# Kernel tuning notes

Hardware: AMD Instinct MI355X
Metric: run time of the kernel (lower is better)

Reference implementation:

```python
import jax, jax.numpy as jnp
import numpy as np

D_MODEL = 1024
NUM_HEADS = 16
D_K = D_MODEL // NUM_HEADS


def setup_inputs() -> dict:
    key = jax.random.key(0)
    ks = jax.random.split(key, 12)
    b, t1, t2 = 4, 2048, 2048
    s = 1.0 / np.sqrt(D_MODEL)
    inp = {
        "q": jax.random.normal(ks[0], (b, t1, D_MODEL), jnp.float32),
        "k": jax.random.normal(ks[1], (b, t2, D_MODEL), jnp.float32),
        "v": jax.random.normal(ks[2], (b, t2, D_MODEL), jnp.float32),
        "mask": jnp.ones((b, 1, 1, t2), dtype=bool),
        "w_q": jax.random.normal(ks[3], (D_MODEL, D_MODEL), jnp.float32) * s,
        "b_q": jax.random.normal(ks[4], (D_MODEL,), jnp.float32) * s,
        "w_k": jax.random.normal(ks[5], (D_MODEL, D_MODEL), jnp.float32) * s,
        "b_k": jax.random.normal(ks[6], (D_MODEL,), jnp.float32) * s,
        "w_v": jax.random.normal(ks[7], (D_MODEL, D_MODEL), jnp.float32) * s,
        "b_v": jax.random.normal(ks[8], (D_MODEL,), jnp.float32) * s,
        "w_o": jax.random.normal(ks[9], (D_MODEL, D_MODEL), jnp.float32) * s,
        "b_o": jax.random.normal(ks[10], (D_MODEL,), jnp.float32) * s,
    }
    return inp


def reference(q, k, v, mask, w_q, b_q, w_k, b_k, w_v, b_v, w_o, b_o):
    b, t1, _ = q.shape
    t2 = k.shape[1]
    # projections -> (b, h, t, d_k)
    qh = (q @ w_q.T + b_q).reshape(b, t1, NUM_HEADS, D_K).transpose(0, 2, 1, 3)
    kh = (k @ w_k.T + b_k).reshape(b, t2, NUM_HEADS, D_K).transpose(0, 2, 1, 3)
    vh = (v @ w_v.T + b_v).reshape(b, t2, NUM_HEADS, D_K).transpose(0, 2, 1, 3)
    scores = jnp.einsum("bhqd,bhkd->bhqk", qh, kh) / jnp.sqrt(
        jnp.asarray(D_K, qh.dtype)
    )
    scores = jnp.where(mask, scores, jnp.asarray(-jnp.inf, scores.dtype))
    attn = jax.nn.softmax(scores, axis=-1)  # dropout_rate=0.0 -> identity
    out = jnp.einsum("bhqk,bhkd->bhqd", attn, vh)
    out = out.transpose(0, 2, 1, 3).reshape(b, t1, D_MODEL)
    return out @ w_o.T + b_o
```

## Files before the change

kernel.cpp:

```cpp
#include <hip/hip_runtime.h>


#define T_SEQ 2048
#define DMODEL 1024
#define NH 16
#define DK 64
#define BATCH 4
#define M_ROWS (BATCH * T_SEQ)

#define OFF_QB (0ull)
#define OFF_KB (8ull << 20)
#define OFF_VB (16ull << 20)
#define OFF_WQ (24ull << 20)
#define OFF_WK (25ull << 20)
#define OFF_WV (26ull << 20)
#define OFF_WO (27ull << 20)
#define OFF_QH (28ull << 20)
#define OFF_KH (36ull << 20)
#define OFF_VT (44ull << 20)
#define OFF_OB (52ull << 20)

typedef short bf16x8 __attribute__((ext_vector_type(8)));
typedef float f32x4 __attribute__((ext_vector_type(4)));

__device__ __forceinline__ unsigned short f2bf(float f) {
  unsigned u = __float_as_uint(f);
  u += 0x7FFFu + ((u >> 16) & 1u);
  return (unsigned short)(u >> 16);
}

__device__ __forceinline__ void async_cp16(void* lds, const void* g) {
  __builtin_amdgcn_global_load_lds(
      (__attribute__((address_space(1))) void*)(void*)g,
      (__attribute__((address_space(3))) void*)lds, 16, 0, 0);
}

__global__ __launch_bounds__(256) void cvt_all(
    const float* __restrict__ q, const float* __restrict__ k,
    const float* __restrict__ v, const float* __restrict__ wq,
    const float* __restrict__ wk, const float* __restrict__ wv,
    const float* __restrict__ wo, unsigned short* __restrict__ ws) {
  const float* src;
  unsigned short* dst;
  int n4;
  switch (blockIdx.y) {
    case 0: src = q;  dst = ws + OFF_QB; n4 = (M_ROWS * DMODEL) / 4; break;
    case 1: src = k;  dst = ws + OFF_KB; n4 = (M_ROWS * DMODEL) / 4; break;
    case 2: src = v;  dst = ws + OFF_VB; n4 = (M_ROWS * DMODEL) / 4; break;
    case 3: src = wq; dst = ws + OFF_WQ; n4 = (DMODEL * DMODEL) / 4; break;
    case 4: src = wk; dst = ws + OFF_WK; n4 = (DMODEL * DMODEL) / 4; break;
    case 5: src = wv; dst = ws + OFF_WV; n4 = (DMODEL * DMODEL) / 4; break;
    default: src = wo; dst = ws + OFF_WO; n4 = (DMODEL * DMODEL) / 4; break;
  }
  int i = blockIdx.x * 256 + threadIdx.x;
  if (i >= n4) return;
  float4 f = ((const float4*)src)[i];
  ushort4 o = make_ushort4(f2bf(f.x), f2bf(f.y), f2bf(f.z), f2bf(f.w));
  ((ushort4*)dst)[i] = o;
}

template <int MODE>
__global__ __launch_bounds__(256) void gemm_bt(
    const unsigned short* __restrict__ A, const unsigned short* __restrict__ W,
    const float* __restrict__ bias, void* __restrict__ outp, float scale) {
  constexpr int K = DMODEL;
  __shared__ unsigned short Al[128 * 32];
  __shared__ unsigned short Bl[128 * 32];
  const int tid = threadIdx.x;
  const int wave = tid >> 6, lane = tid & 63;
  const int quad = lane >> 4, l15 = lane & 15;
  const int m0 = blockIdx.x * 128, n0 = blockIdx.y * 128;
  const int wm0 = (wave >> 1) * 64, wn0 = (wave & 1) * 64;

  f32x4 acc[4][4] = {};

  const unsigned short* Ag = A + (size_t)(m0 + lane) * K + wave * 8;
  const unsigned short* Wg = W + (size_t)(n0 + lane) * K + wave * 8;
  char* AlB = (char*)Al + wave * 2048;
  char* BlB = (char*)Bl + wave * 2048;

  for (int k0 = 0; k0 < K; k0 += 32) {
    async_cp16(AlB, Ag + k0);
    async_cp16(AlB + 1024, Ag + k0 + (size_t)64 * K);
    async_cp16(BlB, Wg + k0);
    async_cp16(BlB + 1024, Wg + k0 + (size_t)64 * K);
    __syncthreads();
    bf16x8 av[4], bv[4];
    const bf16x8* Af = (const bf16x8*)Al;
    const bf16x8* Bf = (const bf16x8*)Bl;
#pragma unroll
    for (int mi = 0; mi < 4; ++mi) av[mi] = Af[quad * 128 + wm0 + mi * 16 + l15];
#pragma unroll
    for (int ni = 0; ni < 4; ++ni) bv[ni] = Bf[quad * 128 + wn0 + ni * 16 + l15];
#pragma unroll
    for (int mi = 0; mi < 4; ++mi)
#pragma unroll
      for (int ni = 0; ni < 4; ++ni)
        acc[mi][ni] = __builtin_amdgcn_mfma_f32_16x16x32_bf16(
            av[mi], bv[ni], acc[mi][ni], 0, 0, 0);
    __syncthreads();
  }

#pragma unroll
  for (int ni = 0; ni < 4; ++ni) {
    const int C = n0 + wn0 + ni * 16 + l15;
    const float bc = bias[C];
#pragma unroll
    for (int mi = 0; mi < 4; ++mi) {
      const int Rbase = m0 + wm0 + mi * 16 + quad * 4;
      if (MODE == 0) {
#pragma unroll
        for (int r = 0; r < 4; ++r) {
          const int R = Rbase + r;
          const float val = (acc[mi][ni][r] + bc) * scale;
          const int bb = R >> 11, t = R & (T_SEQ - 1);
          const int h = C >> 6, d = C & 63;
          ((unsigned short*)outp)[(((size_t)bb * NH + h) * T_SEQ + t) * DK + d] =
              f2bf(val);
        }
      } else if (MODE == 1) {
        const int bb = Rbase >> 11, t = Rbase & (T_SEQ - 1);
        const int h = C >> 6, d = C & 63;
        unsigned short* p =
            (unsigned short*)outp + (((size_t)bb * NH + h) * DK + d) * T_SEQ + t;
        ushort4 pk = make_ushort4(
            f2bf(acc[mi][ni][0] + bc), f2bf(acc[mi][ni][1] + bc),
            f2bf(acc[mi][ni][2] + bc), f2bf(acc[mi][ni][3] + bc));
        *(ushort4*)p = pk;
      } else {
#pragma unroll
        for (int r = 0; r < 4; ++r) {
          const int R = Rbase + r;
          ((float*)outp)[(size_t)R * DMODEL + C] = acc[mi][ni][r] + bc;
        }
      }
    }
  }
}

__global__ __launch_bounds__(256) void attn(
    const unsigned short* __restrict__ Qh, const unsigned short* __restrict__ Kh,
    const unsigned short* __restrict__ Vt, unsigned short* __restrict__ Ob) {
  __shared__ unsigned short Ql[128 * 64];
  __shared__ unsigned short Kl[2][64 * 64];
  __shared__ unsigned short Vl[2][64 * 64];
  __shared__ unsigned short Pl[4][2048];
  const int tid = threadIdx.x, wave = tid >> 6, lane = tid & 63;
  const int quad = lane >> 4, l15 = lane & 15;
  const int t1_0 = blockIdx.x * 128;
  const int bh = blockIdx.y;
  const unsigned short* Qb = Qh + (size_t)bh * T_SEQ * DK;
  const unsigned short* Kb = Kh + (size_t)bh * T_SEQ * DK;
  const unsigned short* Vb = Vt + (size_t)bh * DK * T_SEQ;

  {
    char* qbase = (char*)Ql + wave * 4 * 1024;
#pragma unroll
    for (int i = 0; i < 4; ++i) {
      int s = wave * 4 + i;
      int db = s >> 1, mh = s & 1;
      async_cp16(qbase + i * 1024,
                 Qb + (size_t)(t1_0 + mh * 64 + lane) * DK + db * 8);
    }
  }
  async_cp16((char*)Kl[0] + wave * 1024, Kb + (size_t)lane * DK + wave * 8);
  async_cp16((char*)Kl[0] + (wave + 4) * 1024,
             Kb + (size_t)lane * DK + (wave + 4) * 8);
  async_cp16((char*)Vl[0] + wave * 1024, Vb + (size_t)lane * T_SEQ + wave * 8);
  async_cp16((char*)Vl[0] + (wave + 4) * 1024,
             Vb + (size_t)lane * T_SEQ + (wave + 4) * 8);
  __syncthreads();

  bf16x8 aq[2][2];
#pragma unroll
  for (int mi = 0; mi < 2; ++mi)
#pragma unroll
    for (int kc = 0; kc < 2; ++kc)
      aq[mi][kc] =
          ((const bf16x8*)Ql)[(kc * 4 + quad) * 128 + wave * 32 + mi * 16 + l15];

  float lstate[2][4] = {};
  f32x4 o[2][4] = {};
  unsigned short* Pw = Pl[wave];

  for (int it = 0; it < T_SEQ / 64; ++it) {
    const int buf = it & 1;
    if (it + 1 < T_SEQ / 64) {
      const int t2n = (it + 1) * 64, nb = buf ^ 1;
      async_cp16((char*)Kl[nb] + wave * 1024,
                 Kb + (size_t)(t2n + lane) * DK + wave * 8);
      async_cp16((char*)Kl[nb] + (wave + 4) * 1024,
                 Kb + (size_t)(t2n + lane) * DK + (wave + 4) * 8);
      async_cp16((char*)Vl[nb] + wave * 1024,
                 Vb + (size_t)lane * T_SEQ + t2n + wave * 8);
      async_cp16((char*)Vl[nb] + (wave + 4) * 1024,
                 Vb + (size_t)lane * T_SEQ + t2n + (wave + 4) * 8);
    }

    f32x4 sa[2][4] = {};
#pragma unroll
    for (int kc = 0; kc < 2; ++kc) {
      bf16x8 bk[4];
#pragma unroll
      for (int ni = 0; ni < 4; ++ni)
        bk[ni] = ((const bf16x8*)Kl[buf])[(kc * 4 + quad) * 64 + ni * 16 + l15];
#pragma unroll
      for (int mi = 0; mi < 2; ++mi)
#pragma unroll
        for (int ni = 0; ni < 4; ++ni)
          sa[mi][ni] = __builtin_amdgcn_mfma_f32_16x16x32_bf16(
              aq[mi][kc], bk[ni], sa[mi][ni], 0, 0, 0);
    }

#pragma unroll
    for (int mi = 0; mi < 2; ++mi)
#pragma unroll
      for (int ni = 0; ni < 4; ++ni) {
        const int col = ni * 16 + l15;
        const int chunk = col >> 3, cin = col & 7;
#pragma unroll
        for (int r = 0; r < 4; ++r) {
          const float p = __expf(sa[mi][ni][r]);
          lstate[mi][r] += p;
          const int mrow = mi * 16 + quad * 4 + r;
          Pw[(chunk * 32 + mrow) * 8 + cin] = f2bf(p);
        }
      }

#pragma unroll
    for (int kc = 0; kc < 2; ++kc) {
      bf16x8 vfr[4];
#pragma unroll
      for (int ni = 0; ni < 4; ++ni)
        vfr[ni] = ((const bf16x8*)Vl[buf])[(kc * 4 + quad) * 64 + ni * 16 + l15];
#pragma unroll
      for (int mi = 0; mi < 2; ++mi) {
        bf16x8 pf = ((const bf16x8*)Pw)[(kc * 4 + quad) * 32 + mi * 16 + l15];
#pragma unroll
        for (int ni = 0; ni < 4; ++ni)
          o[mi][ni] = __builtin_amdgcn_mfma_f32_16x16x32_bf16(pf, vfr[ni],
                                                              o[mi][ni], 0, 0, 0);
      }
    }
    __syncthreads();
  }

  const int bb = bh >> 4, h = bh & 15;
#pragma unroll
  for (int mi = 0; mi < 2; ++mi) {
#pragma unroll
    for (int r = 0; r < 4; ++r) {
      float l = lstate[mi][r];
      l += __shfl_xor(l, 1);
      l += __shfl_xor(l, 2);
      l += __shfl_xor(l, 4);
      l += __shfl_xor(l, 8);
      const float inv = 1.f / l;
      const int t = t1_0 + wave * 32 + mi * 16 + quad * 4 + r;
#pragma unroll
      for (int ni = 0; ni < 4; ++ni) {
        const int d = ni * 16 + l15;
        Ob[((size_t)bb * T_SEQ + t) * DMODEL + h * DK + d] =
            f2bf(o[mi][ni][r] * inv);
      }
    }
  }
}

extern "C" void kernel_launch(void* const* d_in, const int* in_sizes, int n_in,
                              void* d_out, int out_size, void* d_ws,
                              size_t ws_size, hipStream_t stream) {
  const float* q = (const float*)d_in[0];
  const float* k = (const float*)d_in[1];
  const float* v = (const float*)d_in[2];
  const float* wq = (const float*)d_in[4];
  const float* bq = (const float*)d_in[5];
  const float* wk = (const float*)d_in[6];
  const float* bk = (const float*)d_in[7];
  const float* wv = (const float*)d_in[8];
  const float* bv = (const float*)d_in[9];
  const float* wo = (const float*)d_in[10];
  const float* bo = (const float*)d_in[11];
  unsigned short* ws = (unsigned short*)d_ws;

  cvt_all<<<dim3(8192, 7), 256, 0, stream>>>(q, k, v, wq, wk, wv, wo, ws);

  gemm_bt<0><<<dim3(64, 8), 256, 0, stream>>>(ws + OFF_QB, ws + OFF_WQ, bq,
                                              ws + OFF_QH, 0.125f);
  gemm_bt<0><<<dim3(64, 8), 256, 0, stream>>>(ws + OFF_KB, ws + OFF_WK, bk,
                                              ws + OFF_KH, 1.0f);
  gemm_bt<1><<<dim3(64, 8), 256, 0, stream>>>(ws + OFF_VB, ws + OFF_WV, bv,
                                              ws + OFF_VT, 1.0f);

  attn<<<dim3(16, 64), 256, 0, stream>>>(ws + OFF_QH, ws + OFF_KH, ws + OFF_VT,
                                         ws + OFF_OB);

  gemm_bt<2><<<dim3(64, 8), 256, 0, stream>>>(ws + OFF_OB, ws + OFF_WO, bo,
                                              d_out, 1.0f);
}
```

Baseline: 443.0 us.

## Keep softmax probabilities in registers, batch QKV GEMMs, remap attention grid

The attention kernel computes S transposed (K as the A operand), so each lane's exp'd probabilities already match the 16x16x16 MFMA operand layout for P·V. This removes the per-wave LDS round trip for P and lets row sums be reduced with fewer shuffles. The three QKV projection GEMMs are merged into one launch using blockIdx.z. Attention now runs on a 1D grid with a swizzled head/tile mapping and a launch bound of 3 blocks per CU. The conversion kernel uses a grid-stride loop with fewer blocks. The smaller 16x16x16 MFMA does half the work per instruction, so it needs twice as many instructions as the previous 16x16x32 form.

```diff
diff --git a/kernel.cpp b/kernel.cpp
--- a/kernel.cpp
+++ b/kernel.cpp
@@ -21,6 +21,7 @@
 #define OFF_OB (52ull << 20)
 
 typedef short bf16x8 __attribute__((ext_vector_type(8)));
+typedef short bf16x4 __attribute__((ext_vector_type(4)));
 typedef float f32x4 __attribute__((ext_vector_type(4)));
 
 __device__ __forceinline__ unsigned short f2bf(float f) {
@@ -52,24 +53,25 @@
     case 5: src = wv; dst = ws + OFF_WV; n4 = (DMODEL * DMODEL) / 4; break;
     default: src = wo; dst = ws + OFF_WO; n4 = (DMODEL * DMODEL) / 4; break;
   }
-  int i = blockIdx.x * 256 + threadIdx.x;
-  if (i >= n4) return;
-  float4 f = ((const float4*)src)[i];
-  ushort4 o = make_ushort4(f2bf(f.x), f2bf(f.y), f2bf(f.z), f2bf(f.w));
-  ((ushort4*)dst)[i] = o;
+  for (int i = blockIdx.x * 256 + threadIdx.x; i < n4; i += gridDim.x * 256) {
+    float4 f = ((const float4*)src)[i];
+    ushort4 o = make_ushort4(f2bf(f.x), f2bf(f.y), f2bf(f.z), f2bf(f.w));
+    ((ushort4*)dst)[i] = o;
+  }
 }
 
 template <int MODE>
-__global__ __launch_bounds__(256) void gemm_bt(
+__device__ __forceinline__ void gemm_core(
     const unsigned short* __restrict__ A, const unsigned short* __restrict__ W,
-    const float* __restrict__ bias, void* __restrict__ outp, float scale) {
+    const float* __restrict__ bias, void* __restrict__ outp, float scale,
+    int bx, int by) {
   constexpr int K = DMODEL;
   __shared__ unsigned short Al[128 * 32];
   __shared__ unsigned short Bl[128 * 32];
   const int tid = threadIdx.x;
   const int wave = tid >> 6, lane = tid & 63;
   const int quad = lane >> 4, l15 = lane & 15;
-  const int m0 = blockIdx.x * 128, n0 = blockIdx.y * 128;
+  const int m0 = bx * 128, n0 = by * 128;
   const int wm0 = (wave >> 1) * 64, wn0 = (wave & 1) * 64;
 
   f32x4 acc[4][4] = {};
@@ -138,17 +140,37 @@
   }
 }
 
-__global__ __launch_bounds__(256) void attn(
+__global__ __launch_bounds__(256) void qkv_gemm(
+    unsigned short* __restrict__ ws, const float* __restrict__ bq,
+    const float* __restrict__ bk, const float* __restrict__ bv) {
+  if (blockIdx.z == 0)
+    gemm_core<0>(ws + OFF_QB, ws + OFF_WQ, bq, ws + OFF_QH, 0.125f,
+                 blockIdx.x, blockIdx.y);
+  else if (blockIdx.z == 1)
+    gemm_core<0>(ws + OFF_KB, ws + OFF_WK, bk, ws + OFF_KH, 1.0f,
+                 blockIdx.x, blockIdx.y);
+  else
+    gemm_core<1>(ws + OFF_VB, ws + OFF_WV, bv, ws + OFF_VT, 1.0f,
+                 blockIdx.x, blockIdx.y);
+}
+
+__global__ __launch_bounds__(256) void oproj_gemm(
+    const unsigned short* __restrict__ A, const unsigned short* __restrict__ W,
+    const float* __restrict__ bias, float* __restrict__ outp) {
+  gemm_core<2>(A, W, bias, outp, 1.0f, blockIdx.x, blockIdx.y);
+}
+
+__global__ __launch_bounds__(256, 3) void attn(
     const unsigned short* __restrict__ Qh, const unsigned short* __restrict__ Kh,
     const unsigned short* __restrict__ Vt, unsigned short* __restrict__ Ob) {
   __shared__ unsigned short Ql[128 * 64];
   __shared__ unsigned short Kl[2][64 * 64];
   __shared__ unsigned short Vl[2][64 * 64];
-  __shared__ unsigned short Pl[4][2048];
   const int tid = threadIdx.x, wave = tid >> 6, lane = tid & 63;
   const int quad = lane >> 4, l15 = lane & 15;
-  const int t1_0 = blockIdx.x * 128;
-  const int bh = blockIdx.y;
+  const int bid = blockIdx.x;
+  const int bh = (bid & 7) * 8 + ((bid >> 3) >> 4);
+  const int t1_0 = ((bid >> 3) & 15) * 128;
   const unsigned short* Qb = Qh + (size_t)bh * T_SEQ * DK;
   const unsigned short* Kb = Kh + (size_t)bh * T_SEQ * DK;
   const unsigned short* Vb = Vt + (size_t)bh * DK * T_SEQ;
@@ -173,15 +195,14 @@
 
   bf16x8 aq[2][2];
 #pragma unroll
-  for (int mi = 0; mi < 2; ++mi)
+  for (int qt = 0; qt < 2; ++qt)
 #pragma unroll
     for (int kc = 0; kc < 2; ++kc)
-      aq[mi][kc] =
-          ((const bf16x8*)Ql)[(kc * 4 + quad) * 128 + wave * 32 + mi * 16 + l15];
-
-  float lstate[2][4] = {};
+      aq[qt][kc] =
+          ((const bf16x8*)Ql)[(kc * 4 + quad) * 128 + wave * 32 + qt * 16 + l15];
+
+  float lstate[2] = {0.f, 0.f};
   f32x4 o[2][4] = {};
-  unsigned short* Pw = Pl[wave];
 
   for (int it = 0; it < T_SEQ / 64; ++it) {
     const int buf = it & 1;
@@ -197,71 +218,72 @@
                  Vb + (size_t)lane * T_SEQ + t2n + (wave + 4) * 8);
     }
 
-    f32x4 sa[2][4] = {};
+    f32x4 sa[4][2] = {};
 #pragma unroll
     for (int kc = 0; kc < 2; ++kc) {
       bf16x8 bk[4];
 #pragma unroll
-      for (int ni = 0; ni < 4; ++ni)
-        bk[ni] = ((const bf16x8*)Kl[buf])[(kc * 4 + quad) * 64 + ni * 16 + l15];
-#pragma unroll
-      for (int mi = 0; mi < 2; ++mi)
-#pragma unroll
-        for (int ni = 0; ni < 4; ++ni)
-          sa[mi][ni] = __builtin_amdgcn_mfma_f32_16x16x32_bf16(
-              aq[mi][kc], bk[ni], sa[mi][ni], 0, 0, 0);
-    }
-
-#pragma unroll
-    for (int mi = 0; mi < 2; ++mi)
-#pragma unroll
-      for (int ni = 0; ni < 4; ++ni) {
-        const int col = ni * 16 + l15;
-        const int chunk = col >> 3, cin = col & 7;
-#pragma unroll
-        for (int r = 0; r < 4; ++r) {
-          const float p = __expf(sa[mi][ni][r]);
-          lstate[mi][r] += p;
-          const int mrow = mi * 16 + quad * 4 + r;
-          Pw[(chunk * 32 + mrow) * 8 + cin] = f2bf(p);
-        }
+      for (int kt = 0; kt < 4; ++kt)
+        bk[kt] = ((const bf16x8*)Kl[buf])[(kc * 4 + quad) * 64 + kt * 16 + l15];
+#pragma unroll
+      for (int kt = 0; kt < 4; ++kt)
+#pragma unroll
+        for (int qt = 0; qt < 2; ++qt)
+          sa[kt][qt] = __builtin_amdgcn_mfma_f32_16x16x32_bf16(
+              bk[kt], aq[qt][kc], sa[kt][qt], 0, 0, 0);
+    }
+
+    bf16x4 pf[4][2];
+#pragma unroll
+    for (int kt = 0; kt < 4; ++kt)
+#pragma unroll
+      for (int qt = 0; qt < 2; ++qt) {
+        float p0 = __expf(sa[kt][qt][0]);
+        float p1 = __expf(sa[kt][qt][1]);
+        float p2 = __expf(sa[kt][qt][2]);
+        float p3 = __expf(sa[kt][qt][3]);
+        lstate[qt] += (p0 + p1) + (p2 + p3);
+        bf16x4 pk = {(short)f2bf(p0), (short)f2bf(p1), (short)f2bf(p2),
+                     (short)f2bf(p3)};
+        pf[kt][qt] = pk;
       }
 
 #pragma unroll
-    for (int kc = 0; kc < 2; ++kc) {
-      bf16x8 vfr[4];
-#pragma unroll
-      for (int ni = 0; ni < 4; ++ni)
-        vfr[ni] = ((const bf16x8*)Vl[buf])[(kc * 4 + quad) * 64 + ni * 16 + l15];
-#pragma unroll
-      for (int mi = 0; mi < 2; ++mi) {
-        bf16x8 pf = ((const bf16x8*)Pw)[(kc * 4 + quad) * 32 + mi * 16 + l15];
-#pragma unroll
-        for (int ni = 0; ni < 4; ++ni)
-          o[mi][ni] = __builtin_amdgcn_mfma_f32_16x16x32_bf16(pf, vfr[ni],
-                                                              o[mi][ni], 0, 0, 0);
-      }
+    for (int s = 0; s < 4; ++s) {
+      bf16x4 vf[4];
+#pragma unroll
+      for (int dt = 0; dt < 4; ++dt)
+        vf[dt] = *(const bf16x4*)((const char*)Vl[buf] +
+                                  ((s * 2 + (quad >> 1)) * 64 + dt * 16 + l15) *
+                                      16 +
+                                  (quad & 1) * 8);
+#pragma unroll
+      for (int qt = 0; qt < 2; ++qt)
+#pragma unroll
+        for (int dt = 0; dt < 4; ++dt)
+          o[qt][dt] = __builtin_amdgcn_mfma_f32_16x16x16bf16_1k(
+              pf[s][qt], vf[dt], o[qt][dt], 0, 0, 0);
     }
     __syncthreads();
   }
 
   const int bb = bh >> 4, h = bh & 15;
 #pragma unroll
-  for (int mi = 0; mi < 2; ++mi) {
+  for (int qt = 0; qt < 2; ++qt) {
+    float l = lstate[qt];
+    l += __shfl_xor(l, 16);
+    l += __shfl_xor(l, 32);
+    float inv[4];
+#pragma unroll
+    for (int r = 0; r < 4; ++r) inv[r] = 1.f / __shfl(l, quad * 4 + r, 16);
 #pragma unroll
     for (int r = 0; r < 4; ++r) {
-      float l = lstate[mi][r];
-      l += __shfl_xor(l, 1);
-      l += __shfl_xor(l, 2);
-      l += __shfl_xor(l, 4);
-      l += __shfl_xor(l, 8);
-      const float inv = 1.f / l;
-      const int t = t1_0 + wave * 32 + mi * 16 + quad * 4 + r;
-#pragma unroll
-      for (int ni = 0; ni < 4; ++ni) {
-        const int d = ni * 16 + l15;
+      const int t = t1_0 + wave * 32 + qt * 16 + quad * 4 + r;
+#pragma unroll
+      for (int dt = 0; dt < 4; ++dt) {
+        const int d = dt * 16 + l15;
         Ob[((size_t)bb * T_SEQ + t) * DMODEL + h * DK + d] =
-            f2bf(o[mi][ni][r] * inv);
+            f2bf(o[qt][dt][r] * inv[r]);
       }
     }
   }
@@ -283,18 +305,13 @@
   const float* bo = (const float*)d_in[11];
   unsigned short* ws = (unsigned short*)d_ws;
 
-  cvt_all<<<dim3(8192, 7), 256, 0, stream>>>(q, k, v, wq, wk, wv, wo, ws);
-
-  gemm_bt<0><<<dim3(64, 8), 256, 0, stream>>>(ws + OFF_QB, ws + OFF_WQ, bq,
-                                              ws + OFF_QH, 0.125f);
-  gemm_bt<0><<<dim3(64, 8), 256, 0, stream>>>(ws + OFF_KB, ws + OFF_WK, bk,
-                                              ws + OFF_KH, 1.0f);
-  gemm_bt<1><<<dim3(64, 8), 256, 0, stream>>>(ws + OFF_VB, ws + OFF_WV, bv,
-                                              ws + OFF_VT, 1.0f);
-
-  attn<<<dim3(16, 64), 256, 0, stream>>>(ws + OFF_QH, ws + OFF_KH, ws + OFF_VT,
-                                         ws + OFF_OB);
-
-  gemm_bt<2><<<dim3(64, 8), 256, 0, stream>>>(ws + OFF_OB, ws + OFF_WO, bo,
-                                              d_out, 1.0f);
-}
+  cvt_all<<<dim3(2048, 7), 256, 0, stream>>>(q, k, v, wq, wk, wv, wo, ws);
+
+  qkv_gemm<<<dim3(64, 8, 3), 256, 0, stream>>>(ws, bq, bk, bv);
+
+  attn<<<dim3(1024), 256, 0, stream>>>(ws + OFF_QH, ws + OFF_KH, ws + OFF_VT,
+                                       ws + OFF_OB);
+
+  oproj_gemm<<<dim3(64, 8), 256, 0, stream>>>(ws + OFF_OB, ws + OFF_WO, bo,
+                                              (float*)d_out);
+}
```

Result: faster. 417.8 us (-5.7%).
